# Optimization experiments

Hardware: AMD Instinct MI355X
Metric: run time of the kernel (lower is better)

Reference implementation:

```python
import jax, jax.numpy as jnp
import numpy as np
import math

N_HEAD = 16
N_KV_HEAD = 4
HEAD_DIM = 128  # n_embed // n_head


def apply_rope(x, omega, offset=0):
    # x: (B, T, H, D); omega: (D//2,) Llama-style inverse frequencies
    T = x.shape[1]
    d2 = x.shape[-1] // 2
    pos = (jnp.arange(T) + offset).astype(x.dtype)
    ang = pos[:, None] * omega[None, :]              # (T, d2)
    cos = jnp.cos(ang)[None, :, None, :]
    sin = jnp.sin(ang)[None, :, None, :]
    x1, x2 = x[..., :d2], x[..., d2:]
    return jnp.concatenate([x1 * cos - x2 * sin, x1 * sin + x2 * cos], axis=-1)


def setup_inputs() -> dict:
    key = jax.random.key(0)
    k1, k2, k3, k4 = jax.random.split(key, 4)
    B, T, C = 2, 2048, 2048
    std = 0.02
    x = jax.random.normal(k1, (B, T, C), dtype=jnp.float32)
    wq = jax.random.normal(k2, (C, C), dtype=jnp.float32) * std
    wkv = jax.random.normal(k3, (C, 2 * N_KV_HEAD * HEAD_DIM), dtype=jnp.float32) * std
    wproj = jax.random.normal(k4, (C, C), dtype=jnp.float32) * std * (2 * 24) ** (-0.5)
    # Llama RoPE frequencies: 1 / 10000^(2i/D)
    omega = (1.0 / (10000.0 ** (jnp.arange(0, HEAD_DIM, 2, dtype=jnp.float32) / HEAD_DIM)))
    return {"x": x, "wq": wq, "wkv": wkv, "wproj": wproj, "omega": omega}


def reference(x, wq, wkv, wproj, omega):
    B, T, C = x.shape
    H, KH, D = N_HEAD, N_KV_HEAD, HEAD_DIM
    G = H // KH  # query heads per kv head

    q = (x @ wq).reshape(B, T, H, D)
    kv = x @ wkv
    k, v = jnp.split(kv, 2, axis=-1)

    q = apply_rope(q, omega, offset=0)
    k = apply_rope(k.reshape(B, T, KH, D), omega, offset=0)
    v = v.reshape(B, T, KH, D)

    # GQA causal attention (no KV expansion: group query heads per kv head)
    qr = q.reshape(B, T, KH, G, D)
    scores = jnp.einsum('bqkgd,bskd->bkgqs', qr, k) / math.sqrt(D)
    causal = jnp.tril(jnp.ones((T, T), dtype=bool))
    scores = jnp.where(causal[None, None, None, :, :], scores, -jnp.inf)
    att = jax.nn.softmax(scores, axis=-1)
    y = jnp.einsum('bkgqs,bskd->bqkgd', att, v).reshape(B, T, C)
    return y @ wproj
```

## Files before the change

kernel.cpp:

```cpp
#include <hip/hip_runtime.h>
#include <hip/hip_bf16.h>

#define B_ 2
#define T_ 2048
#define C_ 2048
#define H_ 16
#define KH_ 4
#define D_ 128

typedef unsigned short ushort_t;
typedef __attribute__((ext_vector_type(8))) short short8;
typedef __attribute__((ext_vector_type(4))) float f32x4;

#define RSQRT_D 0.08838834764831845f
#define L2E 1.4426950408889634f
#define QSCALE (0.08838834764831845f * 1.4426950408889634f)

__device__ __forceinline__ ushort_t f2b(float f) {
  union { float f; unsigned u; } v; v.f = f;
  unsigned r = v.u + 0x7fffu + ((v.u >> 16) & 1u);
  return (ushort_t)(r >> 16);
}
__device__ __forceinline__ float b2f(ushort_t u) {
  union { unsigned u; float f; } v; v.u = ((unsigned)u) << 16;
  return v.f;
}

__device__ __forceinline__ f32x4 mfma16(short8 a, short8 b, f32x4 c) {
  return __builtin_amdgcn_mfma_f32_16x16x32_bf16(a, b, c, 0, 0, 0);
}

__device__ __forceinline__ void async16(const void* g, void* l) {
  __builtin_amdgcn_global_load_lds(
      (const __attribute__((address_space(1))) void*)g,
      (__attribute__((address_space(3))) void*)l, 16, 0, 0);
}

__device__ __forceinline__ unsigned cvtpk(float lo, float hi) {
  unsigned r;
  asm volatile("v_cvt_pk_bf16_f32 %0, %1, %2" : "=v"(r) : "v"(lo), "v"(hi));
  return r;
}


__global__ void convert_f32_bf16(const float* __restrict__ in, ushort_t* __restrict__ out, int n4) {
  int i = blockIdx.x * blockDim.x + threadIdx.x;
  if (i >= n4) return;
  float4 v = ((const float4*)in)[i];
  ushort4 o;
  o.x = f2b(v.x); o.y = f2b(v.y); o.z = f2b(v.z); o.w = f2b(v.w);
  ((ushort4*)out)[i] = o;
}

__global__ void transpose_to_bf16(const float* __restrict__ in, ushort_t* __restrict__ out, int R, int C) {
  __shared__ float tile[32][33];
  int c0 = blockIdx.x * 32, r0 = blockIdx.y * 32;
  int tx = threadIdx.x, ty = threadIdx.y;
#pragma unroll
  for (int i = 0; i < 4; i++) {
    int r = ty + i * 8;
    tile[r][tx] = in[(size_t)(r0 + r) * C + c0 + tx];
  }
  __syncthreads();
#pragma unroll
  for (int i = 0; i < 4; i++) {
    int r = ty + i * 8;
    out[(size_t)(c0 + r) * R + r0 + tx] = f2b(tile[tx][r]);
  }
}

__global__ void rope_tab_k(const float* __restrict__ omega, float2* __restrict__ tab) {
  int idx = blockIdx.x * blockDim.x + threadIdx.x;
  int d = idx & 63;
  int t = idx >> 6;
  float ang = (float)t * omega[d];
  tab[idx] = make_float2(cosf(ang), sinf(ang));
}

__global__ void rope_q_k(const ushort_t* __restrict__ QKVraw, const float2* __restrict__ tab,
                         ushort_t* __restrict__ Qb) {
  int idx = blockIdx.x * blockDim.x + threadIdx.x;
  int d = idx & 63;
  int h = (idx >> 6) & 15;
  int t = (idx >> 10) & 2047;
  int b = idx >> 21;
  size_t in_off = (size_t)(b * 2048 + t) * 3072 + h * 128 + d;
  float x1 = b2f(QKVraw[in_off]);
  float x2 = b2f(QKVraw[in_off + 64]);
  float2 cs = tab[t * 64 + d];
  size_t out_off = ((size_t)(b * 16 + h) * 2048 + t) * 128 + d;
  Qb[out_off] = f2b((x1 * cs.x - x2 * cs.y) * QSCALE);
  Qb[out_off + 64] = f2b((x1 * cs.y + x2 * cs.x) * QSCALE);
}

__global__ void rope_k_k(const ushort_t* __restrict__ QKVraw, const float2* __restrict__ tab,
                         ushort_t* __restrict__ Kb) {
  int idx = blockIdx.x * blockDim.x + threadIdx.x;
  int d = idx & 63;
  int kh = (idx >> 6) & 3;
  int t = (idx >> 8) & 2047;
  int b = idx >> 19;
  size_t in_off = (size_t)(b * 2048 + t) * 3072 + 2048 + kh * 128 + d;
  float x1 = b2f(QKVraw[in_off]);
  float x2 = b2f(QKVraw[in_off + 64]);
  float2 cs = tab[t * 64 + d];
  size_t out_off = ((size_t)(b * 4 + kh) * 2048 + t) * 128 + d;
  Kb[out_off] = f2b(x1 * cs.x - x2 * cs.y);
  Kb[out_off + 64] = f2b(x1 * cs.y + x2 * cs.x);
}

__global__ void v_frag_k(const ushort_t* __restrict__ QKVraw, ushort_t* __restrict__ Vf) {
  int idx = blockIdx.x * blockDim.x + threadIdx.x;
  int lane = idx & 63;
  int n = (idx >> 6) & 7;
  int hv = (idx >> 9) & 1;
  int tile = (idx >> 10) & 31;
  int z = idx >> 15;
  int b = z >> 2, kh = z & 3;
  int lr = lane & 15, lc = lane >> 4;
  int d = n * 16 + lr;
  union { ushort_t u[8]; short8 v; } out;
#pragma unroll
  for (int j = 0; j < 8; j++) {
    int tw = j >> 1, par = j & 1;
    int kl = (hv * 2 + (tw >> 1)) * 16 + lc * 4 + 2 * (tw & 1) + par;
    int t = tile * 64 + kl;
    out.u[j] = QKVraw[(size_t)(b * 2048 + t) * 3072 + 2560 + kh * 128 + d];
  }
  *(short8*)(Vf + (size_t)idx * 8) = out.v;
}

__device__ __forceinline__ void store_out(float* C, size_t idx, float v) { C[idx] = v; }
__device__ __forceinline__ void store_out(ushort_t* C, size_t idx, float v) { C[idx] = f2b(v); }


template <typename OUT_T>
__global__ __launch_bounds__(256) void gemm_bt(const ushort_t* __restrict__ A,
                                               const ushort_t* __restrict__ Bt,
                                               OUT_T* __restrict__ C,
                                               int M, int N, int K) {
  __shared__ __attribute__((aligned(16))) ushort_t As[2][128 * 32];
  __shared__ __attribute__((aligned(16))) ushort_t Bs[2][128 * 32];
  const int tid = threadIdx.x;
  const int lane = tid & 63;
  const int w = tid >> 6;
  const int bm = blockIdx.y, bn = blockIdx.x;
  const int lr = lane & 15, lc = lane >> 4;
  const int wr = (w >> 1) * 64, wc = (w & 1) * 64;
  const ushort_t* Ab = A + (size_t)bm * 128 * K;
  const ushort_t* Bb = Bt + (size_t)bn * 128 * K;
  const int srow = tid >> 2;
  const int scol = (tid & 3) * 8;
  f32x4 acc[4][4];
#pragma unroll
  for (int i = 0; i < 4; i++)
#pragma unroll
    for (int j = 0; j < 4; j++) acc[i][j] = (f32x4)(0.0f);

  async16(Ab + (size_t)srow * K + scol, &As[0][0] + srow * 32 + scol);
  async16(Ab + (size_t)(srow + 64) * K + scol, &As[0][0] + (srow + 64) * 32 + scol);
  async16(Bb + (size_t)srow * K + scol, &Bs[0][0] + srow * 32 + scol);
  async16(Bb + (size_t)(srow + 64) * K + scol, &Bs[0][0] + (srow + 64) * 32 + scol);

  const int nt = K >> 5;
#pragma unroll 2
  for (int t = 0; t < nt - 1; t++) {
    const int cur = t & 1;
    {
      const int k1 = (t + 1) << 5;
      ushort_t* Ad = &As[cur ^ 1][0];
      ushort_t* Bd = &Bs[cur ^ 1][0];
      async16(Ab + (size_t)srow * K + k1 + scol, Ad + srow * 32 + scol);
      async16(Ab + (size_t)(srow + 64) * K + k1 + scol, Ad + (srow + 64) * 32 + scol);
      async16(Bb + (size_t)srow * K + k1 + scol, Bd + srow * 32 + scol);
      async16(Bb + (size_t)(srow + 64) * K + k1 + scol, Bd + (srow + 64) * 32 + scol);
    }
    asm volatile("s_waitcnt vmcnt(4)" ::: "memory");
    __builtin_amdgcn_s_barrier();
    __builtin_amdgcn_sched_barrier(0);
    const ushort_t* Al = &As[cur][0];
    const ushort_t* Bl = &Bs[cur][0];
    short8 af[4], bf[4];
#pragma unroll
    for (int mi = 0; mi < 4; mi++)
      af[mi] = *(const short8*)(Al + (wr + mi * 16 + lr) * 32 + lc * 8);
#pragma unroll
    for (int ni = 0; ni < 4; ni++)
      bf[ni] = *(const short8*)(Bl + (wc + ni * 16 + lr) * 32 + lc * 8);
#pragma unroll
    for (int mi = 0; mi < 4; mi++)
#pragma unroll
      for (int ni = 0; ni < 4; ni++)
        acc[mi][ni] = mfma16(af[mi], bf[ni], acc[mi][ni]);
    asm volatile("" ::: "memory");
    __builtin_amdgcn_s_barrier();
    asm volatile("" ::: "memory");
  }
  {
    const int cur = (nt - 1) & 1;
    asm volatile("s_waitcnt vmcnt(0)" ::: "memory");
    __builtin_amdgcn_s_barrier();
    __builtin_amdgcn_sched_barrier(0);
    const ushort_t* Al = &As[cur][0];
    const ushort_t* Bl = &Bs[cur][0];
    short8 af[4], bf[4];
#pragma unroll
    for (int mi = 0; mi < 4; mi++)
      af[mi] = *(const short8*)(Al + (wr + mi * 16 + lr) * 32 + lc * 8);
#pragma unroll
    for (int ni = 0; ni < 4; ni++)
      bf[ni] = *(const short8*)(Bl + (wc + ni * 16 + lr) * 32 + lc * 8);
#pragma unroll
    for (int mi = 0; mi < 4; mi++)
#pragma unroll
      for (int ni = 0; ni < 4; ni++)
        acc[mi][ni] = mfma16(af[mi], bf[ni], acc[mi][ni]);
  }
#pragma unroll
  for (int mi = 0; mi < 4; mi++) {
#pragma unroll
    for (int ni = 0; ni < 4; ni++) {
      int row = bm * 128 + wr + mi * 16 + lc * 4;
      int col = bn * 128 + wc + ni * 16 + lr;
#pragma unroll
      for (int r = 0; r < 4; r++)
        store_out(C, (size_t)(row + r) * N + col, acc[mi][ni][r]);
    }
  }
}

template <typename OUT_T>
__global__ __launch_bounds__(512, 1) void gemm256(const ushort_t* __restrict__ A,
                                                  const ushort_t* __restrict__ Bt,
                                                  OUT_T* __restrict__ C,
                                                  int M, int N, int K) {
  __shared__ __attribute__((aligned(16))) ushort_t As[2][2][8192];
  __shared__ __attribute__((aligned(16))) ushort_t Bs[2][2][8192];
  const int tid = threadIdx.x;
  const int lane = tid & 63;
  const int w = tid >> 6;
  const int lr = lane & 15, lc = lane >> 4;
  const int wm = w >> 2, wn = w & 3;
  const int nwg = gridDim.x;
  const int cpx = nwg >> 3;
  const int swz = (blockIdx.x & 7) * cpx + (blockIdx.x >> 3);
  const int bnc = N >> 8;
  const int bm = swz / bnc, bn = swz % bnc;
  const ushort_t* Ab = A + (size_t)bm * 256 * K;
  const ushort_t* Bb = Bt + (size_t)bn * 256 * K;
  const int sr0 = tid >> 2, sc0 = tid & 3;
  const int sr1 = 128 + (tid >> 2), sc1 = tid & 3;

  f32x4 acc[8][4];
#pragma unroll
  for (int i = 0; i < 8; i++)
#pragma unroll
    for (int j = 0; j < 4; j++) acc[i][j] = (f32x4)(0.0f);

  auto STAGE = [&](int kt, int hid) {
    const int buf = kt & 1;
    const int kk = hid >> 1;
    const ushort_t* gb = (hid & 1) ? Bb : Ab;
    ushort_t* db = (hid & 1) ? &Bs[buf][kk][0] : &As[buf][kk][0];
    const int kbase = kt * 64 + kk * 32;
    {
      const int lch = sc0 ^ ((sr0 >> 1) & 3);
      async16(gb + (size_t)sr0 * K + kbase + lch * 8, db + (sr0 * 4 + sc0) * 8);
    }
    {
      const int lch = sc1 ^ ((sr1 >> 1) & 3);
      async16(gb + (size_t)sr1 * K + kbase + lch * 8, db + (sr1 * 4 + sc1) * 8);
    }
  };

  const int nt = K >> 6;
  STAGE(0, 0); STAGE(0, 1); STAGE(0, 2); STAGE(0, 3);
  asm volatile("s_waitcnt vmcnt(4)" ::: "memory");
  __builtin_amdgcn_s_barrier();

#pragma unroll 1
  for (int t = 0; t < nt; ++t) {
    const int buf = t & 1;
    const ushort_t* Ak0 = &As[buf][0][0];
    const ushort_t* Ak1 = &As[buf][1][0];
    const ushort_t* Bk0 = &Bs[buf][0][0];
    const ushort_t* Bk1 = &Bs[buf][1][0];
    short8 af[4], bf[4];

#pragma unroll
    for (int nf = 0; nf < 4; nf++) {
      const int row = wn * 64 + nf * 16 + lr;
      bf[nf] = *(const short8*)(Bk0 + row * 32 + ((lc ^ ((row >> 1) & 3)) * 8));
    }
#pragma unroll
    for (int mf = 0; mf < 4; mf++) {
      const int row = wm * 128 + mf * 16 + lr;
      af[mf] = *(const short8*)(Ak0 + row * 32 + ((lc ^ ((row >> 1) & 3)) * 8));
    }
    if (t + 1 < nt) STAGE(t + 1, 0);
    __builtin_amdgcn_s_barrier();
    asm volatile("s_waitcnt lgkmcnt(0)" ::: "memory");
    __builtin_amdgcn_sched_barrier(0);
    __builtin_amdgcn_s_setprio(1);
#pragma unroll
    for (int mf = 0; mf < 4; mf++)
#pragma unroll
      for (int nf = 0; nf < 4; nf++)
        acc[mf][nf] = mfma16(af[mf], bf[nf], acc[mf][nf]);
    __builtin_amdgcn_s_setprio(0);
    __builtin_amdgcn_s_barrier();

#pragma unroll
    for (int mf = 0; mf < 4; mf++) {
      const int row = wm * 128 + 64 + mf * 16 + lr;
      af[mf] = *(const short8*)(Ak0 + row * 32 + ((lc ^ ((row >> 1) & 3)) * 8));
    }
    if (t + 1 < nt) STAGE(t + 1, 1);
    __builtin_amdgcn_s_barrier();
    asm volatile("s_waitcnt lgkmcnt(0)" ::: "memory");
    __builtin_amdgcn_sched_barrier(0);
    __builtin_amdgcn_s_setprio(1);
#pragma unroll
    for (int mf = 0; mf < 4; mf++)
#pragma unroll
      for (int nf = 0; nf < 4; nf++)
        acc[4 + mf][nf] = mfma16(af[mf], bf[nf], acc[4 + mf][nf]);
    __builtin_amdgcn_s_setprio(0);
    if (t + 1 < nt) {
      asm volatile("s_waitcnt vmcnt(4)" ::: "memory");
    } else {
      asm volatile("s_waitcnt vmcnt(0)" ::: "memory");
    }
    __builtin_amdgcn_s_barrier();

#pragma unroll
    for (int nf = 0; nf < 4; nf++) {
      const int row = wn * 64 + nf * 16 + lr;
      bf[nf] = *(const short8*)(Bk1 + row * 32 + ((lc ^ ((row >> 1) & 3)) * 8));
    }
#pragma unroll
    for (int mf = 0; mf < 4; mf++) {
      const int row = wm * 128 + mf * 16 + lr;
      af[mf] = *(const short8*)(Ak1 + row * 32 + ((lc ^ ((row >> 1) & 3)) * 8));
    }
    if (t + 1 < nt) STAGE(t + 1, 2);
    __builtin_amdgcn_s_barrier();
    asm volatile("s_waitcnt lgkmcnt(0)" ::: "memory");
    __builtin_amdgcn_sched_barrier(0);
    __builtin_amdgcn_s_setprio(1);
#pragma unroll
    for (int mf = 0; mf < 4; mf++)
#pragma unroll
      for (int nf = 0; nf < 4; nf++)
        acc[mf][nf] = mfma16(af[mf], bf[nf], acc[mf][nf]);
    __builtin_amdgcn_s_setprio(0);
    __builtin_amdgcn_s_barrier();

#pragma unroll
    for (int mf = 0; mf < 4; mf++) {
      const int row = wm * 128 + 64 + mf * 16 + lr;
      af[mf] = *(const short8*)(Ak1 + row * 32 + ((lc ^ ((row >> 1) & 3)) * 8));
    }
    if (t + 1 < nt) STAGE(t + 1, 3);
    __builtin_amdgcn_s_barrier();
    asm volatile("s_waitcnt lgkmcnt(0)" ::: "memory");
    __builtin_amdgcn_sched_barrier(0);
    __builtin_amdgcn_s_setprio(1);
#pragma unroll
    for (int mf = 0; mf < 4; mf++)
#pragma unroll
      for (int nf = 0; nf < 4; nf++)
        acc[4 + mf][nf] = mfma16(af[mf], bf[nf], acc[4 + mf][nf]);
    __builtin_amdgcn_s_setprio(0);
    if (t + 1 < nt) {
      asm volatile("s_waitcnt vmcnt(4)" ::: "memory");
    }
    __builtin_amdgcn_s_barrier();
  }

#pragma unroll
  for (int mfp = 0; mfp < 8; mfp++) {
#pragma unroll
    for (int nf = 0; nf < 4; nf++) {
      const int row = bm * 256 + wm * 128 + mfp * 16 + lc * 4;
      const int col = bn * 256 + wn * 64 + nf * 16 + lr;
#pragma unroll
      for (int r = 0; r < 4; r++)
        store_out(C, (size_t)(row + r) * N + col, acc[mfp][nf][r]);
    }
  }
}

__global__ __launch_bounds__(256, 2) void attn_k(const ushort_t* __restrict__ Qb,
                                                 const ushort_t* __restrict__ Kb,
                                                 const ushort_t* __restrict__ Vf,
                                                 ushort_t* __restrict__ Yb) {
  __shared__ __attribute__((aligned(16))) ushort_t Ks[2][64 * 128];
  const int tid = threadIdx.x;
  const int lane = tid & 63;
  const int w = tid >> 6;
  const int lr = lane & 15, lc = lane >> 4;
  const int gy = blockIdx.y;
  const int h = gy;
  const int b = blockIdx.z;
  const int kh = h >> 2;
  const int qc = b ? (15 - ((blockIdx.x + gy) & 15)) : ((blockIdx.x + gy) & 15);
  const int q0w = qc * 128 + w * 32;

  const ushort_t* Qp = Qb + (size_t)(b * 16 + h) * T_ * D_;
  const ushort_t* Kp = Kb + (size_t)(b * 4 + kh) * T_ * D_;
  const ushort_t* Vfb = Vf + (size_t)(b * 4 + kh) * 262144;

  const int st_row = tid >> 4;
  const int st_slot = tid & 15;

  short8 qf[2][4];
#pragma unroll
  for (int f = 0; f < 2; f++)
#pragma unroll
    for (int c = 0; c < 4; c++)
      qf[f][c] = *(const short8*)(Qp + (size_t)(q0w + f * 16 + lr) * D_ + c * 32 + lc * 8);

  f32x4 o[2][8];
#pragma unroll
  for (int f = 0; f < 2; f++)
#pragma unroll
    for (int n = 0; n < 8; n++) o[f][n] = (f32x4)(0.0f);
  float m[2] = {-1e30f, -1e30f}, l[2] = {0.0f, 0.0f};

  const int nt = 2 * qc + 2;

#pragma unroll
  for (int i = 0; i < 4; i++) {
    int row = i * 16 + st_row;
    async16(Kp + (size_t)row * D_ + (((st_slot - row) & 15) * 8),
            &Ks[0][0] + row * 128 + st_slot * 8);
  }

#pragma unroll 1
  for (int ti = 0; ti < nt; ti++) {
    __syncthreads();
    const int kv0 = ti * 64;
    if (ti + 1 < nt) {
      const ushort_t* Kn = Kp + (size_t)(kv0 + 64) * D_;
      ushort_t* dst = &Ks[(ti + 1) & 1][0];
#pragma unroll
      for (int i = 0; i < 4; i++) {
        int row = i * 16 + st_row;
        async16(Kn + (size_t)row * D_ + (((st_slot - row) & 15) * 8),
                dst + row * 128 + st_slot * 8);
      }
    }
    if (kv0 > q0w + 31) continue;
    const ushort_t* Kl = &Ks[ti & 1][0];
    const ushort_t* Vt0 = Vfb + (size_t)(ti * 2) * 4096;
    short8 vr0[8];
#pragma unroll
    for (int n = 0; n < 8; n++)
      vr0[n] = *(const short8*)(Vt0 + n * 512 + lane * 8);
    f32x4 s[2][4];
#pragma unroll
    for (int f = 0; f < 2; f++)
#pragma unroll
      for (int kj = 0; kj < 4; kj++) s[f][kj] = (f32x4)(0.0f);
    __builtin_amdgcn_s_setprio(1);
#pragma unroll
    for (int c = 0; c < 4; c++) {
      short8 kf[4];
#pragma unroll
      for (int kj = 0; kj < 4; kj++)
        kf[kj] = *(const short8*)(Kl + (kj * 16 + lr) * 128 + (((c * 4 + lc + lr) & 15) * 8));
#pragma unroll
      for (int f = 0; f < 2; f++)
#pragma unroll
        for (int kj = 0; kj < 4; kj++)
          s[f][kj] = mfma16(kf[kj], qf[f][c], s[f][kj]);
    }
    __builtin_amdgcn_s_setprio(0);
    const ushort_t* Vt1 = Vfb + (size_t)(ti * 2 + 1) * 4096;
    short8 vr1[8];
#pragma unroll
    for (int n = 0; n < 8; n++)
      vr1[n] = *(const short8*)(Vt1 + n * 512 + lane * 8);
    const bool maskt = (kv0 + 63 > q0w);
    union { unsigned u[4]; short8 v; } pa0[2], pa1[2];
#pragma unroll
    for (int f = 0; f < 2; f++) {
      const int q = q0w + f * 16 + lr;
      float pv[16];
      float mx = -1e30f;
      if (maskt) {
#pragma unroll
        for (int kj = 0; kj < 4; kj++)
#pragma unroll
          for (int r = 0; r < 4; r++) {
            float a = s[f][kj][r];
            if (kv0 + kj * 16 + lc * 4 + r > q) a = -1e30f;
            pv[kj * 4 + r] = a;
            mx = fmaxf(mx, a);
          }
      } else {
#pragma unroll
        for (int kj = 0; kj < 4; kj++)
#pragma unroll
          for (int r = 0; r < 4; r++) {
            float a = s[f][kj][r];
            pv[kj * 4 + r] = a;
            mx = fmaxf(mx, a);
          }
      }
      mx = fmaxf(mx, __shfl_xor(mx, 16));
      mx = fmaxf(mx, __shfl_xor(mx, 32));
      const bool need = __any(mx > m[f] + 8.0f);
      const float mn = need ? fmaxf(m[f], mx) : m[f];
      float rs = 0.0f;
#pragma unroll
      for (int i = 0; i < 16; i++) {
        pv[i] = exp2f(pv[i] - mn);
        rs += pv[i];
      }
      rs += __shfl_xor(rs, 16);
      rs += __shfl_xor(rs, 32);
#pragma unroll
      for (int kj = 0; kj < 2; kj++) {
        pa0[f].u[kj * 2] = cvtpk(pv[kj * 4], pv[kj * 4 + 1]);
        pa0[f].u[kj * 2 + 1] = cvtpk(pv[kj * 4 + 2], pv[kj * 4 + 3]);
        pa1[f].u[kj * 2] = cvtpk(pv[8 + kj * 4], pv[8 + kj * 4 + 1]);
        pa1[f].u[kj * 2 + 1] = cvtpk(pv[8 + kj * 4 + 2], pv[8 + kj * 4 + 3]);
      }
      if (need) {
        float al = exp2f(m[f] - mn);
        m[f] = mn;
        l[f] = l[f] * al + rs;
        float alT[4];
#pragma unroll
        for (int r = 0; r < 4; r++)
          alT[r] = __shfl(al, (lane & 48) | (lc * 4 + r));
#pragma unroll
        for (int n = 0; n < 8; n++)
#pragma unroll
          for (int r = 0; r < 4; r++) o[f][n][r] *= alT[r];
      } else {
        l[f] += rs;
      }
    }
    __builtin_amdgcn_s_setprio(1);
#pragma unroll
    for (int n = 0; n < 8; n++) {
      o[0][n] = mfma16(pa0[0].v, vr0[n], o[0][n]);
      o[1][n] = mfma16(pa0[1].v, vr0[n], o[1][n]);
    }
#pragma unroll
    for (int n = 0; n < 8; n++) {
      o[0][n] = mfma16(pa1[0].v, vr1[n], o[0][n]);
      o[1][n] = mfma16(pa1[1].v, vr1[n], o[1][n]);
    }
    __builtin_amdgcn_s_setprio(0);
  }
#pragma unroll
  for (int f = 0; f < 2; f++) {
    float inv = 1.0f / l[f];
    float invT[4];
#pragma unroll
    for (int r = 0; r < 4; r++)
      invT[r] = __shfl(inv, (lane & 48) | (lc * 4 + r));
#pragma unroll
    for (int n = 0; n < 8; n++)
#pragma unroll
      for (int r = 0; r < 4; r++) {
        int qo = q0w + f * 16 + lc * 4 + r;
        int d = n * 16 + lr;
        Yb[(size_t)(b * T_ + qo) * 2048 + h * 128 + d] = f2b(o[f][n][r] * invT[r]);
      }
  }
}


extern "C" void kernel_launch(void* const* d_in, const int* in_sizes, int n_in,
                              void* d_out, int out_size, void* d_ws, size_t ws_size,
                              hipStream_t stream) {
  (void)in_sizes; (void)n_in; (void)out_size; (void)ws_size;
  const float* x = (const float*)d_in[0];
  const float* wq = (const float*)d_in[1];
  const float* wkv = (const float*)d_in[2];
  const float* wproj = (const float*)d_in[3];
  const float* omega = (const float*)d_in[4];
  float* out = (float*)d_out;
  char* ws = (char*)d_ws;

  ushort_t* xb     = (ushort_t*)(ws + 0);
  ushort_t* wqkvT  = (ushort_t*)(ws + 16777216);
  ushort_t* wkvT   = (ushort_t*)(ws + 25165824);
  ushort_t* wprojT = (ushort_t*)(ws + 29360128);
  ushort_t* QKVraw = (ushort_t*)(ws + 37748736);
  ushort_t* Qb     = (ushort_t*)(ws + 62914560);
  ushort_t* Kb     = (ushort_t*)(ws + 79691776);
  ushort_t* Vf     = (ushort_t*)(ws + 83886080);
  ushort_t* Yb     = (ushort_t*)(ws + 88080384);
  float2*   tab    = (float2*)(ws + 104857600);

  convert_f32_bf16<<<8192, 256, 0, stream>>>(x, xb, 2097152);
  transpose_to_bf16<<<dim3(64, 64), dim3(32, 8), 0, stream>>>(wq, wqkvT, 2048, 2048);
  transpose_to_bf16<<<dim3(32, 64), dim3(32, 8), 0, stream>>>(wkv, wkvT, 2048, 1024);
  transpose_to_bf16<<<dim3(64, 64), dim3(32, 8), 0, stream>>>(wproj, wprojT, 2048, 2048);
  rope_tab_k<<<512, 256, 0, stream>>>(omega, tab);

  gemm256<<<192, 512, 0, stream>>>(xb, wqkvT, QKVraw, 4096, 3072, 2048);

  rope_q_k<<<16384, 256, 0, stream>>>(QKVraw, tab, Qb);
  rope_k_k<<<4096, 256, 0, stream>>>(QKVraw, tab, Kb);
  v_frag_k<<<1024, 256, 0, stream>>>(QKVraw, Vf);

  attn_k<<<dim3(16, 16, 2), 256, 0, stream>>>(Qb, Kb, Vf, Yb);

  gemm_bt<<<dim3(16, 32), 256, 0, stream>>>(Yb, wprojT, out, 4096, 2048, 2048);
}
```

Baseline: 221.3 us.

## Use 256x192 QKV GEMM tiles for full CU coverage and vectorize RoPE kernels

The QKV GEMM tile changes from 256x256 to 256x192, so the grid grows from 192 to 256 workgroups and better fills the GPU's compute units. Each wave now covers 48 columns, and some threads issue dummy async loads into a scratch buffer so the per-thread async-copy counts stay uniform for the vmcnt waits. Separately, the RoPE kernels for Q and K now process four elements per thread with vectorized ushort4/float4 loads and stores, cutting thread count and memory transactions. The smaller N tile lowers MFMA reuse per loaded A fragment, and the dummy loads add some extra memory traffic.

```diff
diff --git a/kernel.cpp b/kernel.cpp
--- a/kernel.cpp
+++ b/kernel.cpp
@@ -80,33 +80,53 @@
 __global__ void rope_q_k(const ushort_t* __restrict__ QKVraw, const float2* __restrict__ tab,
                          ushort_t* __restrict__ Qb) {
   int idx = blockIdx.x * blockDim.x + threadIdx.x;
-  int d = idx & 63;
-  int h = (idx >> 6) & 15;
-  int t = (idx >> 10) & 2047;
-  int b = idx >> 21;
-  size_t in_off = (size_t)(b * 2048 + t) * 3072 + h * 128 + d;
-  float x1 = b2f(QKVraw[in_off]);
-  float x2 = b2f(QKVraw[in_off + 64]);
-  float2 cs = tab[t * 64 + d];
-  size_t out_off = ((size_t)(b * 16 + h) * 2048 + t) * 128 + d;
-  Qb[out_off] = f2b((x1 * cs.x - x2 * cs.y) * QSCALE);
-  Qb[out_off + 64] = f2b((x1 * cs.y + x2 * cs.x) * QSCALE);
+  int d4 = (idx & 15) * 4;
+  int h = (idx >> 4) & 15;
+  int t = (idx >> 8) & 2047;
+  int b = idx >> 19;
+  size_t in_off = (size_t)(b * 2048 + t) * 3072 + h * 128 + d4;
+  ushort4 x1 = *(const ushort4*)(QKVraw + in_off);
+  ushort4 x2 = *(const ushort4*)(QKVraw + in_off + 64);
+  float4 csA = *(const float4*)(&tab[t * 64 + d4]);
+  float4 csB = *(const float4*)(&tab[t * 64 + d4 + 2]);
+  ushort4 o1, o2;
+  o1.x = f2b((b2f(x1.x) * csA.x - b2f(x2.x) * csA.y) * QSCALE);
+  o2.x = f2b((b2f(x1.x) * csA.y + b2f(x2.x) * csA.x) * QSCALE);
+  o1.y = f2b((b2f(x1.y) * csA.z - b2f(x2.y) * csA.w) * QSCALE);
+  o2.y = f2b((b2f(x1.y) * csA.w + b2f(x2.y) * csA.z) * QSCALE);
+  o1.z = f2b((b2f(x1.z) * csB.x - b2f(x2.z) * csB.y) * QSCALE);
+  o2.z = f2b((b2f(x1.z) * csB.y + b2f(x2.z) * csB.x) * QSCALE);
+  o1.w = f2b((b2f(x1.w) * csB.z - b2f(x2.w) * csB.w) * QSCALE);
+  o2.w = f2b((b2f(x1.w) * csB.w + b2f(x2.w) * csB.z) * QSCALE);
+  size_t out_off = ((size_t)(b * 16 + h) * 2048 + t) * 128 + d4;
+  *(ushort4*)(Qb + out_off) = o1;
+  *(ushort4*)(Qb + out_off + 64) = o2;
 }
 
 __global__ void rope_k_k(const ushort_t* __restrict__ QKVraw, const float2* __restrict__ tab,
                          ushort_t* __restrict__ Kb) {
   int idx = blockIdx.x * blockDim.x + threadIdx.x;
-  int d = idx & 63;
-  int kh = (idx >> 6) & 3;
-  int t = (idx >> 8) & 2047;
-  int b = idx >> 19;
-  size_t in_off = (size_t)(b * 2048 + t) * 3072 + 2048 + kh * 128 + d;
-  float x1 = b2f(QKVraw[in_off]);
-  float x2 = b2f(QKVraw[in_off + 64]);
-  float2 cs = tab[t * 64 + d];
-  size_t out_off = ((size_t)(b * 4 + kh) * 2048 + t) * 128 + d;
-  Kb[out_off] = f2b(x1 * cs.x - x2 * cs.y);
-  Kb[out_off + 64] = f2b(x1 * cs.y + x2 * cs.x);
+  int d4 = (idx & 15) * 4;
+  int kh = (idx >> 4) & 3;
+  int t = (idx >> 6) & 2047;
+  int b = idx >> 17;
+  size_t in_off = (size_t)(b * 2048 + t) * 3072 + 2048 + kh * 128 + d4;
+  ushort4 x1 = *(const ushort4*)(QKVraw + in_off);
+  ushort4 x2 = *(const ushort4*)(QKVraw + in_off + 64);
+  float4 csA = *(const float4*)(&tab[t * 64 + d4]);
+  float4 csB = *(const float4*)(&tab[t * 64 + d4 + 2]);
+  ushort4 o1, o2;
+  o1.x = f2b(b2f(x1.x) * csA.x - b2f(x2.x) * csA.y);
+  o2.x = f2b(b2f(x1.x) * csA.y + b2f(x2.x) * csA.x);
+  o1.y = f2b(b2f(x1.y) * csA.z - b2f(x2.y) * csA.w);
+  o2.y = f2b(b2f(x1.y) * csA.w + b2f(x2.y) * csA.z);
+  o1.z = f2b(b2f(x1.z) * csB.x - b2f(x2.z) * csB.y);
+  o2.z = f2b(b2f(x1.z) * csB.y + b2f(x2.z) * csB.x);
+  o1.w = f2b(b2f(x1.w) * csB.z - b2f(x2.w) * csB.w);
+  o2.w = f2b(b2f(x1.w) * csB.w + b2f(x2.w) * csB.z);
+  size_t out_off = ((size_t)(b * 4 + kh) * 2048 + t) * 128 + d4;
+  *(ushort4*)(Kb + out_off) = o1;
+  *(ushort4*)(Kb + out_off + 64) = o2;
 }
 
 __global__ void v_frag_k(const ushort_t* __restrict__ QKVraw, ushort_t* __restrict__ Vf) {
@@ -235,7 +255,8 @@
                                                   OUT_T* __restrict__ C,
                                                   int M, int N, int K) {
   __shared__ __attribute__((aligned(16))) ushort_t As[2][2][8192];
-  __shared__ __attribute__((aligned(16))) ushort_t Bs[2][2][8192];
+  __shared__ __attribute__((aligned(16))) ushort_t Bs[2][2][6144];
+  __shared__ __attribute__((aligned(16))) ushort_t Scr[512];
   const int tid = threadIdx.x;
   const int lane = tid & 63;
   const int w = tid >> 6;
@@ -244,32 +265,47 @@
   const int nwg = gridDim.x;
   const int cpx = nwg >> 3;
   const int swz = (blockIdx.x & 7) * cpx + (blockIdx.x >> 3);
-  const int bnc = N >> 8;
+  const int bnc = N / 192;
   const int bm = swz / bnc, bn = swz % bnc;
   const ushort_t* Ab = A + (size_t)bm * 256 * K;
-  const ushort_t* Bb = Bt + (size_t)bn * 256 * K;
-  const int sr0 = tid >> 2, sc0 = tid & 3;
-  const int sr1 = 128 + (tid >> 2), sc1 = tid & 3;
-
-  f32x4 acc[8][4];
+  const ushort_t* Bb = Bt + (size_t)bn * 192 * K;
+
+  f32x4 acc[8][3];
 #pragma unroll
   for (int i = 0; i < 8; i++)
 #pragma unroll
-    for (int j = 0; j < 4; j++) acc[i][j] = (f32x4)(0.0f);
+    for (int j = 0; j < 3; j++) acc[i][j] = (f32x4)(0.0f);
 
   auto STAGE = [&](int kt, int hid) {
     const int buf = kt & 1;
     const int kk = hid >> 1;
-    const ushort_t* gb = (hid & 1) ? Bb : Ab;
-    ushort_t* db = (hid & 1) ? &Bs[buf][kk][0] : &As[buf][kk][0];
     const int kbase = kt * 64 + kk * 32;
-    {
-      const int lch = sc0 ^ ((sr0 >> 1) & 3);
-      async16(gb + (size_t)sr0 * K + kbase + lch * 8, db + (sr0 * 4 + sc0) * 8);
-    }
-    {
-      const int lch = sc1 ^ ((sr1 >> 1) & 3);
-      async16(gb + (size_t)sr1 * K + kbase + lch * 8, db + (sr1 * 4 + sc1) * 8);
+    if (!(hid & 1)) {
+      ushort_t* db = &As[buf][kk][0];
+      {
+        const int u = tid, row = u >> 2, c = u & 3;
+        const int lch = c ^ ((row >> 1) & 3);
+        async16(Ab + (size_t)row * K + kbase + lch * 8, db + u * 8);
+      }
+      {
+        const int u = 512 + tid, row = u >> 2, c = u & 3;
+        const int lch = c ^ ((row >> 1) & 3);
+        async16(Ab + (size_t)row * K + kbase + lch * 8, db + u * 8);
+      }
+    } else {
+      ushort_t* db = &Bs[buf][kk][0];
+      {
+        const int u = tid, row = u >> 2, c = u & 3;
+        const int lch = c ^ ((row >> 1) & 3);
+        async16(Bb + (size_t)row * K + kbase + lch * 8, db + u * 8);
+      }
+      if (tid < 256) {
+        const int u = 512 + tid, row = u >> 2, c = u & 3;
+        const int lch = c ^ ((row >> 1) & 3);
+        async16(Bb + (size_t)row * K + kbase + lch * 8, db + u * 8);
+      } else {
+        async16(Bb + (size_t)(tid - 256) * 8, &Scr[0]);
+      }
     }
   };
 
@@ -285,11 +321,11 @@
     const ushort_t* Ak1 = &As[buf][1][0];
     const ushort_t* Bk0 = &Bs[buf][0][0];
     const ushort_t* Bk1 = &Bs[buf][1][0];
-    short8 af[4], bf[4];
-
-#pragma unroll
-    for (int nf = 0; nf < 4; nf++) {
-      const int row = wn * 64 + nf * 16 + lr;
+    short8 af[4], bf[3];
+
+#pragma unroll
+    for (int nf = 0; nf < 3; nf++) {
+      const int row = wn * 48 + nf * 16 + lr;
       bf[nf] = *(const short8*)(Bk0 + row * 32 + ((lc ^ ((row >> 1) & 3)) * 8));
     }
 #pragma unroll
@@ -305,7 +341,7 @@
 #pragma unroll
     for (int mf = 0; mf < 4; mf++)
 #pragma unroll
-      for (int nf = 0; nf < 4; nf++)
+      for (int nf = 0; nf < 3; nf++)
         acc[mf][nf] = mfma16(af[mf], bf[nf], acc[mf][nf]);
     __builtin_amdgcn_s_setprio(0);
     __builtin_amdgcn_s_barrier();
@@ -323,7 +359,7 @@
 #pragma unroll
     for (int mf = 0; mf < 4; mf++)
 #pragma unroll
-      for (int nf = 0; nf < 4; nf++)
+      for (int nf = 0; nf < 3; nf++)
         acc[4 + mf][nf] = mfma16(af[mf], bf[nf], acc[4 + mf][nf]);
     __builtin_amdgcn_s_setprio(0);
     if (t + 1 < nt) {
@@ -334,8 +370,8 @@
     __builtin_amdgcn_s_barrier();
 
 #pragma unroll
-    for (int nf = 0; nf < 4; nf++) {
-      const int row = wn * 64 + nf * 16 + lr;
+    for (int nf = 0; nf < 3; nf++) {
+      const int row = wn * 48 + nf * 16 + lr;
       bf[nf] = *(const short8*)(Bk1 + row * 32 + ((lc ^ ((row >> 1) & 3)) * 8));
     }
 #pragma unroll
@@ -351,7 +387,7 @@
 #pragma unroll
     for (int mf = 0; mf < 4; mf++)
 #pragma unroll
-      for (int nf = 0; nf < 4; nf++)
+      for (int nf = 0; nf < 3; nf++)
         acc[mf][nf] = mfma16(af[mf], bf[nf], acc[mf][nf]);
     __builtin_amdgcn_s_setprio(0);
     __builtin_amdgcn_s_barrier();
@@ -369,7 +405,7 @@
 #pragma unroll
     for (int mf = 0; mf < 4; mf++)
 #pragma unroll
-      for (int nf = 0; nf < 4; nf++)
+      for (int nf = 0; nf < 3; nf++)
         acc[4 + mf][nf] = mfma16(af[mf], bf[nf], acc[4 + mf][nf]);
     __builtin_amdgcn_s_setprio(0);
     if (t + 1 < nt) {
@@ -381,9 +417,9 @@
 #pragma unroll
   for (int mfp = 0; mfp < 8; mfp++) {
 #pragma unroll
-    for (int nf = 0; nf < 4; nf++) {
+    for (int nf = 0; nf < 3; nf++) {
       const int row = bm * 256 + wm * 128 + mfp * 16 + lc * 4;
-      const int col = bn * 256 + wn * 64 + nf * 16 + lr;
+      const int col = bn * 192 + wn * 48 + nf * 16 + lr;
 #pragma unroll
       for (int r = 0; r < 4; r++)
         store_out(C, (size_t)(row + r) * N + col, acc[mfp][nf][r]);
@@ -605,10 +641,10 @@
   transpose_to_bf16<<<dim3(64, 64), dim3(32, 8), 0, stream>>>(wproj, wprojT, 2048, 2048);
   rope_tab_k<<<512, 256, 0, stream>>>(omega, tab);
 
-  gemm256<<<192, 512, 0, stream>>>(xb, wqkvT, QKVraw, 4096, 3072, 2048);
-
-  rope_q_k<<<16384, 256, 0, stream>>>(QKVraw, tab, Qb);
-  rope_k_k<<<4096, 256, 0, stream>>>(QKVraw, tab, Kb);
+  gemm256<<<256, 512, 0, stream>>>(xb, wqkvT, QKVraw, 4096, 3072, 2048);
+
+  rope_q_k<<<4096, 256, 0, stream>>>(QKVraw, tab, Qb);
+  rope_k_k<<<1024, 256, 0, stream>>>(QKVraw, tab, Kb);
   v_frag_k<<<1024, 256, 0, stream>>>(QKVraw, Vf);
 
   attn_k<<<dim3(16, 16, 2), 256, 0, stream>>>(Qb, Kb, Vf, Yb);
```

Measured after the change: 216.2 us. -2.3%, faster.
